# Kernel optimization log

Hardware: AMD Instinct MI355X
Metric: run time of the kernel (lower is better)

## Reference

```python
import jax, jax.numpy as jnp
import numpy as np

B, N, T, N_IN = 4, 40, 64, 4
N_EMB, N_HID = 32, 64
EPS = 1e-05


def _spatial_rels(n):
    # fully-connected directed edges without self-loops (NRI convention)
    offdiag = np.ones((n, n)) - np.eye(n)
    recv_idx, send_idx = np.where(offdiag)[0], np.where(offdiag)[1]
    eye = np.eye(n, dtype=np.float32)
    return eye[recv_idx], eye[send_idx]  # [n*(n-1), n] each


def _temporal_rels(t):
    # all t*t ordered pairs (including self), one-hot
    eye = np.eye(t, dtype=np.float32)
    recv = np.repeat(np.arange(t), t)
    send = np.tile(np.arange(t), t)
    return eye[recv], eye[send]  # [t*t, t] each


def setup_inputs() -> dict:
    key = jax.random.key(0)
    ks = jax.random.split(key, 8)
    rel_rec, rel_send = _spatial_rels(N)
    rel_rec_t, rel_send_t = _temporal_rels(T)
    s_emb = 1.0 / np.sqrt(N_IN)
    s_lstm = 1.0 / np.sqrt(N_HID)
    s_att = 1.0 / np.sqrt(2 * N_HID)
    return {
        "inputs": jax.random.normal(ks[0], (B, N, T, N_IN), dtype=jnp.float32),
        "rel_rec": jnp.asarray(rel_rec),
        "rel_send": jnp.asarray(rel_send),
        "rel_rec_t": jnp.asarray(rel_rec_t),
        "rel_send_t": jnp.asarray(rel_send_t),
        "W_emb": jax.random.uniform(ks[1], (N_EMB, N_IN), jnp.float32, -s_emb, s_emb),
        "b_emb": jnp.zeros((N_EMB,), jnp.float32),
        "W_ih": jax.random.uniform(ks[2], (4 * N_HID, N_EMB), jnp.float32, -s_lstm, s_lstm),
        "W_hh": jax.random.uniform(ks[3], (4 * N_HID, N_HID), jnp.float32, -s_lstm, s_lstm),
        "b_ih": jax.random.uniform(ks[4], (4 * N_HID,), jnp.float32, -s_lstm, s_lstm),
        "b_hh": jax.random.uniform(ks[5], (4 * N_HID,), jnp.float32, -s_lstm, s_lstm),
        "W_att": jax.random.uniform(ks[6], (1, 2 * N_HID), jnp.float32, -s_att, s_att),
        "b_att": jnp.zeros((1,), jnp.float32),
    }


def _forward(inputs, rel_rec, rel_send, rel_rec_t, rel_send_t,
             W_emb, b_emb, W_ih, W_hh, b_ih, b_hh, W_att, b_att):
    b, n, t, _ = inputs.shape
    nh = W_hh.shape[1]
    locs = inputs[..., :2]

    # ---- LSTMEncoder: per-timestep embedding + LSTM cell (scan over time) ----
    emb = jnp.einsum("bnti,ei->bnte", inputs, W_emb) + b_emb       # [B,N,T,n_emb]
    xs = emb.transpose(2, 0, 1, 3).reshape(t, b * n, -1)            # [T,BN,n_emb]

    def step(carry, x):
        h, c = carry
        gates = x @ W_ih.T + b_ih + h @ W_hh.T + b_hh               # [BN,4H]
        i_g, f_g, g_g, o_g = jnp.split(gates, 4, axis=-1)           # torch gate order i,f,g,o
        i_g = jax.nn.sigmoid(i_g)
        f_g = jax.nn.sigmoid(f_g)
        g_g = jnp.tanh(g_g)
        o_g = jax.nn.sigmoid(o_g)
        c = f_g * c + i_g * g_g
        h = o_g * jnp.tanh(c)
        return (h, c), h

    h0 = jnp.zeros((b * n, nh), inputs.dtype)
    _, hs_t = jax.lax.scan(step, (h0, h0), xs)                      # [T,BN,H]
    hs = hs_t.transpose(1, 0, 2).reshape(b, n, t, nh)               # [B,N,T,H]

    # ---- SoftAttention over timesteps ----
    hsf = hs.reshape(b * n, t, nh)                                  # [BN,T,H]
    senders = jnp.einsum("kt,mth->mkh", rel_send_t, hsf)            # [BN,T*T,H]
    receivers = jnp.einsum("kt,mth->mkh", rel_rec_t, hsf)
    edges = jnp.concatenate([senders, receivers], axis=-1)          # [BN,T*T,2H]
    scores = jnp.einsum("mkf,of->mko", edges, W_att)[..., 0] + b_att[0]  # [BN,T*T]
    # adj = rel_send_t^T @ diag(scores) @ rel_rec_t (done without diag_embed)
    adj_s = jnp.einsum("ki,mk,kj->mij", rel_send_t, scores, rel_rec_t)   # [BN,T,T]
    adj_sn = jax.nn.softmax(adj_s, axis=-1)
    cs = jnp.einsum("mij,mjh->mih", adj_sn, hsf).reshape(b, n, t, nh)    # [B,N,T,H]

    # ---- HardwiredAttention over atoms ----
    locs_re = locs.reshape(b, n, -1)                                 # [B,N,T*2]
    snd = jnp.einsum("en,bnf->bef", rel_send, locs_re).reshape(b, -1, t, 2)
    rcv = jnp.einsum("en,bnf->bef", rel_rec, locs_re).reshape(b, -1, t, 2)
    dist = jnp.sqrt(((snd - rcv) ** 2).sum(-1))                      # [B,E,T]
    w = (1.0 / (dist + EPS)).transpose(0, 2, 1)                      # [B,T,E]
    adj_h = jnp.einsum("ei,bte,ej->btij", rel_send, w, rel_rec)      # [B,T,N,N]
    ch = jnp.einsum("btij,btjh->btih", adj_h, hs.transpose(0, 2, 1, 3))
    ch = ch.transpose(0, 2, 1, 3)                                    # [B,N,T,H]

    c_out = jnp.tanh(jnp.concatenate([cs[:, :, -1, :], ch.sum(2)], axis=-1))  # [B,N,2H]
    return c_out


def reference(inputs, rel_rec, rel_send, rel_rec_t, rel_send_t,
              W_emb, b_emb, W_ih, W_hh, b_ih, b_hh, W_att, b_att):
    return _forward(inputs, rel_rec, rel_send, rel_rec_t, rel_send_t,
                    W_emb, b_emb, W_ih, W_hh, b_ih, b_hh, W_att, b_att)
```

## Files before the change

kernel.cpp:

```cpp
#include <hip/hip_runtime.h>
#include <math.h>

#define BB   4
#define NN   40
#define TT   64
#define NIN  4
#define NEMB 32
#define NHID 64
#define NG   256
#define EPSW 1e-5f

__global__ __launch_bounds__(256)
void k_lstm(const float* __restrict__ inputs,
            const float* __restrict__ W_emb,
            const float* __restrict__ b_emb,
            const float* __restrict__ W_ih,
            const float* __restrict__ W_hh,
            const float* __restrict__ b_ih,
            const float* __restrict__ b_hh,
            const float* __restrict__ W_att,
            float* __restrict__ out,
            float* __restrict__ hs_g)
{
    __shared__ __align__(16) float s_x[TT * NIN];
    __shared__ __align__(16) float s_emb[TT * NEMB];
    __shared__ __align__(16) float s_act[NG];
    __shared__ __align__(16) float s_h[NHID];
    __shared__ __align__(16) float s_hs[TT * (NHID + 1)];
    __shared__ __align__(16) float s_war[NHID];
    __shared__ __align__(16) float s_p[TT];

    const int m   = blockIdx.x;
    const int tid = threadIdx.x;
    const int g   = tid;
    const int gtype = g >> 6;

    s_x[tid] = inputs[m * (TT * NIN) + tid];
    if (tid < NHID) s_war[tid] = W_att[NHID + tid];
    __syncthreads();

    for (int idx = tid; idx < TT * NEMB; idx += 256) {
        const int t = idx >> 5;
        const int e = idx & 31;
        float v = b_emb[e];
        #pragma unroll
        for (int i = 0; i < NIN; ++i)
            v += s_x[t * NIN + i] * W_emb[e * NIN + i];
        s_emb[idx] = v;
    }

    float wih[NEMB];
    float whh[NHID];
    {
        const float4* p4 = (const float4*)(W_ih + g * NEMB);
        #pragma unroll
        for (int k = 0; k < NEMB / 4; ++k) {
            float4 v = p4[k];
            wih[4 * k + 0] = v.x; wih[4 * k + 1] = v.y;
            wih[4 * k + 2] = v.z; wih[4 * k + 3] = v.w;
        }
        const float4* q4 = (const float4*)(W_hh + g * NHID);
        #pragma unroll
        for (int k = 0; k < NHID / 4; ++k) {
            float4 v = q4[k];
            whh[4 * k + 0] = v.x; whh[4 * k + 1] = v.y;
            whh[4 * k + 2] = v.z; whh[4 * k + 3] = v.w;
        }
    }
    const float bias = b_ih[g] + b_hh[g];

    if (tid < NHID) s_h[tid] = 0.0f;
    float c = 0.0f;
    __syncthreads();

    for (int t = 0; t < TT; ++t) {
        float v0 = bias, v1 = 0.f, v2 = 0.f, v3 = 0.f;
        const float4* e4 = (const float4*)(s_emb + t * NEMB);
        #pragma unroll
        for (int k = 0; k < NEMB / 4; ++k) {
            float4 a = e4[k];
            v0 += a.x * wih[4 * k + 0];
            v1 += a.y * wih[4 * k + 1];
            v2 += a.z * wih[4 * k + 2];
            v3 += a.w * wih[4 * k + 3];
        }
        const float4* h4 = (const float4*)s_h;
        #pragma unroll
        for (int k = 0; k < NHID / 4; ++k) {
            float4 a = h4[k];
            v0 += a.x * whh[4 * k + 0];
            v1 += a.y * whh[4 * k + 1];
            v2 += a.z * whh[4 * k + 2];
            v3 += a.w * whh[4 * k + 3];
        }
        const float v = (v0 + v1) + (v2 + v3);

        float a;
        if (gtype == 2) a = tanhf(v);
        else            a = 1.0f / (1.0f + expf(-v));
        s_act[g] = a;
        __syncthreads();

        if (tid < NHID) {
            const float ig = s_act[tid];
            const float fg = s_act[NHID + tid];
            const float gg = s_act[2 * NHID + tid];
            const float og = s_act[3 * NHID + tid];
            c = fg * c + ig * gg;
            const float h = og * tanhf(c);
            s_h[tid] = h;
            s_hs[t * (NHID + 1) + tid] = h;
            hs_g[(m * TT + t) * NHID + tid] = h;
        }
        __syncthreads();
    }

    if (tid < TT) {
        const int t = tid;
        float r = 0.0f;
        #pragma unroll
        for (int k = 0; k < NHID; ++k)
            r += s_hs[t * (NHID + 1) + k] * s_war[k];
        float mx = r;
        #pragma unroll
        for (int off = 32; off >= 1; off >>= 1)
            mx = fmaxf(mx, __shfl_xor(mx, off));
        const float e = expf(r - mx);
        float s = e;
        #pragma unroll
        for (int off = 32; off >= 1; off >>= 1)
            s += __shfl_xor(s, off);
        s_p[t] = e / s;
    }
    __syncthreads();

    if (tid < NHID) {
        const int h = tid;
        float acc = 0.0f;
        #pragma unroll
        for (int t = 0; t < TT; ++t)
            acc += s_p[t] * s_hs[t * (NHID + 1) + h];
        out[m * (2 * NHID) + h] = tanhf(acc);
    }
}

__global__ __launch_bounds__(256)
void k_spatial(const float* __restrict__ inputs,
               const float* __restrict__ hs_g,
               float* __restrict__ out)
{
    __shared__ float s_w[TT * NN];
    __shared__ float s_part[4 * NHID];

    const int bi  = blockIdx.x;
    const int b   = bi / NN;
    const int i   = bi - b * NN;
    const int tid = threadIdx.x;

    for (int idx = tid; idx < TT * NN; idx += 256) {
        const int t = idx / NN;
        const int j = idx - t * NN;
        const float* pi = inputs + ((b * NN + i) * TT + t) * NIN;
        const float* pj = inputs + ((b * NN + j) * TT + t) * NIN;
        const float dx = pi[0] - pj[0];
        const float dy = pi[1] - pj[1];
        const float d  = sqrtf(dx * dx + dy * dy);
        s_w[idx] = (j == i) ? 0.0f : 1.0f / (d + EPSW);
    }
    __syncthreads();

    const int h = tid & 63;
    const int q = tid >> 6;

    const float* base = hs_g + (size_t)b * NN * TT * NHID + h;
    float a0 = 0.f, a1 = 0.f, a2 = 0.f, a3 = 0.f;
    for (int t = q * 16; t < q * 16 + 16; ++t) {
        const float* hp = base + t * NHID;
        const float* wp = s_w + t * NN;
        #pragma unroll
        for (int j = 0; j < NN; j += 4) {
            a0 += wp[j + 0] * hp[(size_t)(j + 0) * TT * NHID];
            a1 += wp[j + 1] * hp[(size_t)(j + 1) * TT * NHID];
            a2 += wp[j + 2] * hp[(size_t)(j + 2) * TT * NHID];
            a3 += wp[j + 3] * hp[(size_t)(j + 3) * TT * NHID];
        }
    }
    s_part[q * NHID + h] = (a0 + a1) + (a2 + a3);
    __syncthreads();

    if (tid < NHID) {
        const float s = s_part[tid] + s_part[NHID + tid] +
                        s_part[2 * NHID + tid] + s_part[3 * NHID + tid];
        out[bi * (2 * NHID) + NHID + tid] = tanhf(s);
    }
}

extern "C" void kernel_launch(void* const* d_in, const int* in_sizes, int n_in,
                              void* d_out, int out_size, void* d_ws, size_t ws_size,
                              hipStream_t stream) {
    const float* inputs = (const float*)d_in[0];
    const float* W_emb  = (const float*)d_in[5];
    const float* b_emb  = (const float*)d_in[6];
    const float* W_ih   = (const float*)d_in[7];
    const float* W_hh   = (const float*)d_in[8];
    const float* b_ih   = (const float*)d_in[9];
    const float* b_hh   = (const float*)d_in[10];
    const float* W_att  = (const float*)d_in[11];

    float* outp = (float*)d_out;
    float* hs_g = (float*)d_ws;

    hipLaunchKernelGGL(k_lstm, dim3(BB * NN), dim3(256), 0, stream,
                       inputs, W_emb, b_emb, W_ih, W_hh, b_ih, b_hh, W_att,
                       outp, hs_g);
    hipLaunchKernelGGL(k_spatial, dim3(BB * NN), dim3(256), 0, stream,
                       inputs, hs_g, outp);
}
```

Before: 146.6 us.

## Fold embedding into LSTM input weights, halve barriers, use fast math

Folds the linear embedding into the LSTM input projection, giving a 4-wide per-gate weight, and precomputes all 64 input-gate contributions in registers before the recurrence. The cell update is now done redundantly by all four wavefronts, with double-buffered activations, so each timestep needs one barrier instead of two. The global hs stores move out of the loop into a coalesced copy afterwards. tanh, sigmoid, exp and divide switch to fast intrinsics, which lowers accuracy slightly, and the 64-entry register array plus full unroll raise register pressure.

```diff
diff --git a/kernel.cpp b/kernel.cpp
--- a/kernel.cpp
+++ b/kernel.cpp
@@ -9,6 +9,13 @@
 #define NHID 64
 #define NG   256
 #define EPSW 1e-5f
+
+__device__ __forceinline__ float fast_sigmoid(float x) {
+    return __fdividef(1.0f, 1.0f + __expf(-x));
+}
+__device__ __forceinline__ float fast_tanh(float x) {
+    return __fdividef(2.0f, 1.0f + __expf(-2.0f * x)) - 1.0f;
+}
 
 __global__ __launch_bounds__(256)
 void k_lstm(const float* __restrict__ inputs,
@@ -23,9 +30,8 @@
             float* __restrict__ hs_g)
 {
     __shared__ __align__(16) float s_x[TT * NIN];
-    __shared__ __align__(16) float s_emb[TT * NEMB];
-    __shared__ __align__(16) float s_act[NG];
     __shared__ __align__(16) float s_h[NHID];
+    __shared__ __align__(16) float s_act[2][NG];
     __shared__ __align__(16) float s_hs[TT * (NHID + 1)];
     __shared__ __align__(16) float s_war[NHID];
     __shared__ __align__(16) float s_p[TT];
@@ -33,32 +39,35 @@
     const int m   = blockIdx.x;
     const int tid = threadIdx.x;
     const int g   = tid;
+    const int j   = tid & 63;
     const int gtype = g >> 6;
 
     s_x[tid] = inputs[m * (TT * NIN) + tid];
-    if (tid < NHID) s_war[tid] = W_att[NHID + tid];
-    __syncthreads();
-
-    for (int idx = tid; idx < TT * NEMB; idx += 256) {
-        const int t = idx >> 5;
-        const int e = idx & 31;
-        float v = b_emb[e];
-        #pragma unroll
-        for (int i = 0; i < NIN; ++i)
-            v += s_x[t * NIN + i] * W_emb[e * NIN + i];
-        s_emb[idx] = v;
-    }
-
-    float wih[NEMB];
+    if (tid < NHID) { s_war[tid] = W_att[NHID + tid]; s_h[tid] = 0.0f; }
+
+    float wcx = 0.f, wcy = 0.f, wcz = 0.f, wcw = 0.f;
+    float bc  = b_ih[g] + b_hh[g];
+    {
+        const float4* wih4  = (const float4*)(W_ih + g * NEMB);
+        const float4* wemb4 = (const float4*)W_emb;
+        #pragma unroll
+        for (int e4 = 0; e4 < NEMB / 4; ++e4) {
+            float4 wv = wih4[e4];
+            float4 m0 = wemb4[4 * e4 + 0];
+            float4 m1 = wemb4[4 * e4 + 1];
+            float4 m2 = wemb4[4 * e4 + 2];
+            float4 m3 = wemb4[4 * e4 + 3];
+            wcx += wv.x * m0.x + wv.y * m1.x + wv.z * m2.x + wv.w * m3.x;
+            wcy += wv.x * m0.y + wv.y * m1.y + wv.z * m2.y + wv.w * m3.y;
+            wcz += wv.x * m0.z + wv.y * m1.z + wv.z * m2.z + wv.w * m3.z;
+            wcw += wv.x * m0.w + wv.y * m1.w + wv.z * m2.w + wv.w * m3.w;
+            bc  += wv.x * b_emb[4 * e4 + 0] + wv.y * b_emb[4 * e4 + 1]
+                 + wv.z * b_emb[4 * e4 + 2] + wv.w * b_emb[4 * e4 + 3];
+        }
+    }
+
     float whh[NHID];
     {
-        const float4* p4 = (const float4*)(W_ih + g * NEMB);
-        #pragma unroll
-        for (int k = 0; k < NEMB / 4; ++k) {
-            float4 v = p4[k];
-            wih[4 * k + 0] = v.x; wih[4 * k + 1] = v.y;
-            wih[4 * k + 2] = v.z; wih[4 * k + 3] = v.w;
-        }
         const float4* q4 = (const float4*)(W_hh + g * NHID);
         #pragma unroll
         for (int k = 0; k < NHID / 4; ++k) {
@@ -67,23 +76,24 @@
             whh[4 * k + 2] = v.z; whh[4 * k + 3] = v.w;
         }
     }
-    const float bias = b_ih[g] + b_hh[g];
-
-    if (tid < NHID) s_h[tid] = 0.0f;
+
+    __syncthreads();
+
+    float gxv[TT];
+    {
+        const float4* x4 = (const float4*)s_x;
+        #pragma unroll
+        for (int t = 0; t < TT; ++t) {
+            float4 x = x4[t];
+            gxv[t] = bc + x.x * wcx + x.y * wcy + x.z * wcz + x.w * wcw;
+        }
+    }
+
     float c = 0.0f;
-    __syncthreads();
-
+    #pragma unroll
     for (int t = 0; t < TT; ++t) {
-        float v0 = bias, v1 = 0.f, v2 = 0.f, v3 = 0.f;
-        const float4* e4 = (const float4*)(s_emb + t * NEMB);
-        #pragma unroll
-        for (int k = 0; k < NEMB / 4; ++k) {
-            float4 a = e4[k];
-            v0 += a.x * wih[4 * k + 0];
-            v1 += a.y * wih[4 * k + 1];
-            v2 += a.z * wih[4 * k + 2];
-            v3 += a.w * wih[4 * k + 3];
-        }
+        const int p = t & 1;
+        float v0 = gxv[t], v1 = 0.f, v2 = 0.f, v3 = 0.f;
         const float4* h4 = (const float4*)s_h;
         #pragma unroll
         for (int k = 0; k < NHID / 4; ++k) {
@@ -94,25 +104,25 @@
             v3 += a.w * whh[4 * k + 3];
         }
         const float v = (v0 + v1) + (v2 + v3);
-
-        float a;
-        if (gtype == 2) a = tanhf(v);
-        else            a = 1.0f / (1.0f + expf(-v));
-        s_act[g] = a;
+        const float a = (gtype == 2) ? fast_tanh(v) : fast_sigmoid(v);
+        s_act[p][g] = a;
         __syncthreads();
 
-        if (tid < NHID) {
-            const float ig = s_act[tid];
-            const float fg = s_act[NHID + tid];
-            const float gg = s_act[2 * NHID + tid];
-            const float og = s_act[3 * NHID + tid];
-            c = fg * c + ig * gg;
-            const float h = og * tanhf(c);
-            s_h[tid] = h;
-            s_hs[t * (NHID + 1) + tid] = h;
-            hs_g[(m * TT + t) * NHID + tid] = h;
-        }
-        __syncthreads();
+        const float ig = s_act[p][j];
+        const float fg = s_act[p][NHID + j];
+        const float gg = s_act[p][2 * NHID + j];
+        const float og = s_act[p][3 * NHID + j];
+        c = fg * c + ig * gg;
+        const float h = og * fast_tanh(c);
+        s_h[j] = h;
+        if (tid < NHID) s_hs[t * (NHID + 1) + j] = h;
+    }
+    __syncthreads();
+
+    #pragma unroll
+    for (int idx = tid; idx < TT * NHID; idx += 256) {
+        const int t = idx >> 6, h = idx & 63;
+        hs_g[m * (TT * NHID) + idx] = s_hs[t * (NHID + 1) + h];
     }
 
     if (tid < TT) {
@@ -125,22 +135,21 @@
         #pragma unroll
         for (int off = 32; off >= 1; off >>= 1)
             mx = fmaxf(mx, __shfl_xor(mx, off));
-        const float e = expf(r - mx);
+        const float e = __expf(r - mx);
         float s = e;
         #pragma unroll
         for (int off = 32; off >= 1; off >>= 1)
             s += __shfl_xor(s, off);
-        s_p[t] = e / s;
+        s_p[t] = __fdividef(e, s);
     }
     __syncthreads();
 
     if (tid < NHID) {
-        const int h = tid;
         float acc = 0.0f;
         #pragma unroll
         for (int t = 0; t < TT; ++t)
-            acc += s_p[t] * s_hs[t * (NHID + 1) + h];
-        out[m * (2 * NHID) + h] = tanhf(acc);
+            acc += s_p[t] * s_hs[t * (NHID + 1) + tid];
+        out[m * (2 * NHID) + tid] = fast_tanh(acc);
     }
 }
 
@@ -165,7 +174,7 @@
         const float dx = pi[0] - pj[0];
         const float dy = pi[1] - pj[1];
         const float d  = sqrtf(dx * dx + dy * dy);
-        s_w[idx] = (j == i) ? 0.0f : 1.0f / (d + EPSW);
+        s_w[idx] = (j == i) ? 0.0f : __fdividef(1.0f, d + EPSW);
     }
     __syncthreads();
 
@@ -191,7 +200,7 @@
     if (tid < NHID) {
         const float s = s_part[tid] + s_part[NHID + tid] +
                         s_part[2 * NHID + tid] + s_part[3 * NHID + tid];
-        out[bi * (2 * NHID) + NHID + tid] = tanhf(s);
+        out[bi * (2 * NHID) + NHID + tid] = fast_tanh(s);
     }
 }
 
```

Result: no change. 146.7 us (+0.0%).
